# Kernel optimization log

Measured on AMD Instinct MI355X. Metric: run time of the kernel, lower is better.

## Reference

```python
import jax, jax.numpy as jnp
import numpy as np

N = 100000
E = 1600000
NFEAT, NHID, NCLASS = 128, 64, 40
EPS = 1e-5


def _sage_conv(x, src, dst, wl, wr, b):
    # mean aggregation over in-neighbors: out[dst] = mean_{src->dst} x[src]
    msg = jax.ops.segment_sum(x[src], dst, num_segments=N)          # [N, d]
    deg = jax.ops.segment_sum(jnp.ones((src.shape[0],), x.dtype), dst, num_segments=N)
    agg = msg / jnp.maximum(deg, 1.0)[:, None]
    return agg @ wl + x @ wr + b


def _bn_eval(x, g, b, m, v):
    return (x - m) * (g * jax.lax.rsqrt(v + EPS)) + b


def setup_inputs() -> dict:
    key = jax.random.key(0)
    ks = jax.random.split(key, 12)
    s = 0.05
    x = jax.random.normal(ks[0], (N, NFEAT), dtype=jnp.float32)
    edge_index = jax.random.randint(ks[1], (2, E), 0, N, dtype=jnp.int64)
    inp = {
        'x': x,
        'edge_index': edge_index,
        'w1l': jax.random.normal(ks[2], (NFEAT, NHID), jnp.float32) * s,
        'w1r': jax.random.normal(ks[3], (NFEAT, NHID), jnp.float32) * s,
        'b1': jnp.zeros((NHID,), jnp.float32),
        'wxl': jax.random.normal(ks[4], (NHID, NHID), jnp.float32) * s,
        'wxr': jax.random.normal(ks[5], (NHID, NHID), jnp.float32) * s,
        'bx': jnp.zeros((NHID,), jnp.float32),
        'w2l': jax.random.normal(ks[6], (NHID, NCLASS), jnp.float32) * s,
        'w2r': jax.random.normal(ks[7], (NHID, NCLASS), jnp.float32) * s,
        'b2': jnp.zeros((NCLASS,), jnp.float32),
        'bn3_g': jnp.ones((NHID,), jnp.float32),
        'bn3_b': jnp.zeros((NHID,), jnp.float32),
        'bn3_m': jax.random.normal(ks[8], (NHID,), jnp.float32) * 0.1,
        'bn3_v': jax.random.uniform(ks[9], (NHID,), jnp.float32, 0.5, 1.5),
        'bn2_g': jnp.ones((NCLASS,), jnp.float32),
        'bn2_b': jnp.zeros((NCLASS,), jnp.float32),
        'bn2_m': jax.random.normal(ks[10], (NCLASS,), jnp.float32) * 0.1,
        'bn2_v': jax.random.uniform(ks[11], (NCLASS,), jnp.float32, 0.5, 1.5),
    }
    return inp


def reference(x, edge_index, w1l, w1r, b1, wxl, wxr, bx, w2l, w2r, b2,
              bn3_g, bn3_b, bn3_m, bn3_v, bn2_g, bn2_b, bn2_m, bn2_v):
    src, dst = edge_index[0], edge_index[1]
    h = jax.nn.relu(_sage_conv(x, src, dst, w1l, w1r, b1))          # conv1 + relu
    # middle layer (layer=3 -> one convx iteration); dropout = identity (eval)
    h = _sage_conv(h, src, dst, wxl, wxr, bx)
    h = jax.nn.relu(_bn_eval(h, bn3_g, bn3_b, bn3_m, bn3_v))
    # final layer
    h = _sage_conv(h, src, dst, w2l, w2r, b2)
    return _bn_eval(h, bn2_g, bn2_b, bn2_m, bn2_v)                  # [N, NCLASS]
```

## Files before the change

kernel.cpp:

```cpp
#include <hip/hip_runtime.h>

#define NNODES 100000
#define NEDGES 1600000
#define NBK    196
#define BK_CAP 9000
#define BKP    17024
#define CHUNK  4096
#define ZOFF   (NNODES * 128)

typedef short bhalf8 __attribute__((ext_vector_type(8)));
typedef float f32x4 __attribute__((ext_vector_type(4)));

__device__ __forceinline__ unsigned fbits(float x){ union{float f;unsigned u;}c; c.f=x; return c.u; }
__device__ __forceinline__ float bcast(unsigned u){ union{float f;unsigned u;}c; c.u=u; return c.f; }
__device__ __forceinline__ unsigned short rtn16(float x){
    unsigned u = fbits(x);
    return (unsigned short)((u + 0x7FFFu + ((u >> 16) & 1u)) >> 16);
}

__global__ __launch_bounds__(256) void bucketize(
    const int* __restrict__ ei, unsigned* __restrict__ recs, int* __restrict__ bcur) {
    __shared__ int s_is64;
    __shared__ int cnt[256], base[256], loc[256], rnk[256];
    __shared__ unsigned stage[CHUNK];
    __shared__ unsigned char bkof[CHUNK];
    const int t = threadIdx.x;
    if (t < 64) {
        int v = ei[2 * t + 1];
        unsigned long long nz = __ballot(v != 0);
        if (t == 0) s_is64 = (nz == 0ULL) ? 1 : 0;
    }
    cnt[t] = 0; rnk[t] = 0;
    __syncthreads();
    const int is64 = s_is64;
    const long start = (long)blockIdx.x * CHUNK;
    const int2* ei2 = (const int2*)ei;
#pragma unroll
    for (int k = 0; k < CHUNK / 256; ++k) {
        long e = start + k * 256 + t;
        if (e < NEDGES) {
            int d = is64 ? ei2[NEDGES + e].x : ei[NEDGES + e];
            atomicAdd(&cnt[d >> 9], 1);
        }
    }
    __syncthreads();
    int v = cnt[t];
    int run = v;
    loc[t] = run;
    __syncthreads();
    for (int off = 1; off < 256; off <<= 1) {
        int other = (t >= off) ? loc[t - off] : 0;
        __syncthreads();
        run += other;
        loc[t] = run;
        __syncthreads();
    }
    int excl = run - v;
    if (v > 0) base[t] = atomicAdd(&bcur[t], v);
    loc[t] = excl;
    __syncthreads();
#pragma unroll
    for (int k = 0; k < CHUNK / 256; ++k) {
        long e = start + k * 256 + t;
        if (e < NEDGES) {
            int s = is64 ? ei2[e].x : ei[e];
            int d = is64 ? ei2[NEDGES + e].x : ei[NEDGES + e];
            int b = d >> 9;
            int r = atomicAdd(&rnk[b], 1);
            int pos = loc[b] + r;
            stage[pos] = ((unsigned)s << 9) | (unsigned)(d & 511);
            bkof[pos] = (unsigned char)b;
        }
    }
    __syncthreads();
    const int tot = (int)min((long)CHUNK, NEDGES - start);
    for (int i = t; i < tot; i += 256) {
        int b = bkof[i];
        int pos = base[b] + (i - loc[b]);
        if (pos < BK_CAP)
            recs[(size_t)b * BK_CAP + pos] = stage[i];
    }
}

__global__ __launch_bounds__(512) void csr_build(
    const unsigned* __restrict__ recs, const int* __restrict__ bcur,
    int2* __restrict__ offs2, int* __restrict__ degs, int* __restrict__ csr) {
    const int b = blockIdx.x;
    const int t = threadIdx.x;
    const int lo = b << 9;
    __shared__ int sc[512];
    __shared__ int hist[512];
    __shared__ int lstart[512];
    const int n = bcur[b];
    const unsigned* P = recs + (size_t)b * BK_CAP;
    hist[t] = 0;
    __syncthreads();
    for (int i = t; i < n; i += 512)
        atomicAdd(&hist[P[i] & 511], 1);
    __syncthreads();
    const int deg = hist[t];
    const int pad = (deg + 15) & ~15;
    int run = pad;
    sc[t] = run;
    __syncthreads();
    for (int off = 1; off < 512; off <<= 1) {
        int other = (t >= off) ? sc[t - off] : 0;
        __syncthreads();
        run += other;
        sc[t] = run;
        __syncthreads();
    }
    const int start = b * BKP + (run - pad);
    lstart[t] = start;
    const int node = lo + t;
    if (node < NNODES) {
        offs2[node] = make_int2(start, start + pad);
        degs[node] = deg;
    }
    hist[t] = 0;
    __syncthreads();
    for (int i = t; i < n; i += 512) {
        unsigned rec = P[i];
        int d = rec & 511;
        int r = atomicAdd(&hist[d], 1);
        csr[lstart[d] + r] = (int)(rec >> 9) * 128;
    }
    __syncthreads();
    for (int i = deg; i < pad; ++i)
        csr[start + i] = ZOFF;
}

template <int K, int NL, int NTOT>
__device__ __forceinline__ void prep_section(
    int blk, int nblk, const float* wl, const float* wr, const float* bias,
    const float* g, const float* bb, const float* m, const float* vv,
    unsigned short* Bh, unsigned short* Bl, float* bfix) {
    constexpr int NCT = NTOT / 16;
    constexpr int TOT = (K / 32) * NCT * 512;
    int tid = blk * 256 + threadIdx.x;
    if (tid < NL) {
        float sc = g ? g[tid] * rsqrtf(vv[tid] + 1e-5f) : 1.f;
        float sh = g ? (bb[tid] - m[tid] * sc) : 0.f;
        bfix[tid] = bias[tid] * sc + sh;
    }
    for (int idx = tid; idx < TOT; idx += nblk * 256) {
        int e = idx & 7, l = (idx >> 3) & 63, rest = idx >> 9;
        int ct = rest % NCT, kc = rest / NCT;
        int k = kc * 32 + (l >> 4) * 8 + e;
        int j = ct * 16 + (l & 15);
        int jj = (j < NL) ? j : j - NL;
        float sc = g ? g[jj] * rsqrtf(vv[jj] + 1e-5f) : 1.f;
        float v = ((j < NL) ? wl[k * NL + j] : wr[k * NL + (j - NL)]) * sc;
        unsigned short h = rtn16(v);
        float r1 = v - bcast((unsigned)h << 16);
        Bh[idx] = h;
        Bl[idx] = rtn16(r1);
    }
}

__global__ __launch_bounds__(256) void prep_all(
    const float* w1l, const float* w1r, const float* b1,
    const float* wxl, const float* wxr, const float* bx,
    const float* w2l, const float* w2r, const float* b2,
    const float* g3, const float* bb3, const float* m3, const float* v3,
    const float* g2, const float* bb2, const float* m2, const float* v2,
    unsigned short* B1h, unsigned short* B1l, float* bf1,
    unsigned short* B2h, unsigned short* B2l, float* bf2,
    unsigned short* B3h, unsigned short* B3l, float* bf3) {
    int blk = blockIdx.x;
    if (blk < 64)
        prep_section<128, 64, 128>(blk, 64, w1l, w1r, b1,
                                   nullptr, nullptr, nullptr, nullptr, B1h, B1l, bf1);
    else if (blk < 96)
        prep_section<64, 64, 128>(blk - 64, 32, wxl, wxr, bx,
                                  g3, bb3, m3, v3, B2h, B2l, bf2);
    else
        prep_section<64, 40, 80>(blk - 96, 20, w2l, w2r, b2,
                                 g2, bb2, m2, v2, B3h, B3l, bf3);
}

template <int K, int NL, int NTOT, bool ABF16>
__global__ __launch_bounds__(256) void gemm_mfma(
    const void* __restrict__ hvp, const unsigned short* __restrict__ Bh,
    const unsigned short* __restrict__ Bl, const float* __restrict__ bias,
    unsigned short* __restrict__ zl, unsigned short* __restrict__ zr, int nrows) {
    constexpr int NCT = NTOT / 16;
    constexpr int NKC = K / 32;
    int t = threadIdx.x;
    int l = t & 63, w = t >> 6;
    int rb = blockIdx.x * 64 + w * 16;
    int arow = rb + (l & 15);
    int kg = l >> 4;
    f32x4 acc[NCT];
#pragma unroll
    for (int ct = 0; ct < NCT; ++ct) acc[ct] = (f32x4){0.f, 0.f, 0.f, 0.f};
    const bool aok = (arow < nrows);
#pragma unroll
    for (int kc = 0; kc < NKC; ++kc) {
        bhalf8 ah = {0,0,0,0,0,0,0,0}, al = {0,0,0,0,0,0,0,0};
        if (ABF16) {
            const unsigned short* hr =
                (const unsigned short*)hvp + (long)arow * K + kg * 8;
            if (aok) ah = *(const bhalf8*)(hr + kc * 32);
        } else {
            const float* hr = (const float*)hvp + (long)arow * K + kg * 8;
            float4 a0 = make_float4(0.f, 0.f, 0.f, 0.f), a1 = a0;
            if (aok) {
                a0 = *(const float4*)(hr + kc * 32);
                a1 = *(const float4*)(hr + kc * 32 + 4);
            }
            float av[8] = {a0.x, a0.y, a0.z, a0.w, a1.x, a1.y, a1.z, a1.w};
#pragma unroll
            for (int e = 0; e < 8; ++e) {
                unsigned short hh = rtn16(av[e]);
                float r1 = av[e] - bcast((unsigned)hh << 16);
                ah[e] = (short)hh;
                al[e] = (short)rtn16(r1);
            }
        }
        const unsigned short* hp = Bh + (size_t)(kc * NCT) * 512 + l * 8;
        const unsigned short* lp = Bl + (size_t)(kc * NCT) * 512 + l * 8;
#pragma unroll
        for (int ct = 0; ct < NCT; ++ct) {
            bhalf8 bh = *(const bhalf8*)(hp + ct * 512);
            bhalf8 bl = *(const bhalf8*)(lp + ct * 512);
            acc[ct] = __builtin_amdgcn_mfma_f32_16x16x32_bf16(ah, bh, acc[ct], 0, 0, 0);
            acc[ct] = __builtin_amdgcn_mfma_f32_16x16x32_bf16(ah, bl, acc[ct], 0, 0, 0);
            if (!ABF16)
                acc[ct] = __builtin_amdgcn_mfma_f32_16x16x32_bf16(al, bh, acc[ct], 0, 0, 0);
        }
    }
    int orow0 = rb + kg * 4;
#pragma unroll
    for (int ct = 0; ct < NCT; ++ct) {
        int j = ct * 16 + (l & 15);
        bool isl = (j < NL);
        int cc = isl ? j : j - NL;
        float bj = isl ? 0.f : bias[cc];
#pragma unroll
        for (int r = 0; r < 4; ++r) {
            int orow = orow0 + r;
            if (orow < nrows) {
                if (isl) zl[(long)orow * 64 + cc] = rtn16(acc[ct][r]);
                else     zr[(long)orow * NL + cc] = rtn16(acc[ct][r] + bj);
            } else if (orow == nrows && isl) {
                zl[(long)orow * 64 + cc] = 0;
            }
        }
    }
}

template <int NOUT, bool RELU, typename OUTT>
__global__ __launch_bounds__(256) void combine_kernel(
    const unsigned short* __restrict__ zl, const unsigned short* __restrict__ zr,
    const int2* __restrict__ offs2, const int* __restrict__ degs,
    const int* __restrict__ csr, OUTT* __restrict__ out) {
    int wid  = (blockIdx.x * blockDim.x + threadIdx.x) >> 6;
    int lane = threadIdx.x & 63;
    if (wid >= NNODES) return;
    int q    = lane >> 5;
    int li2  = (lane & 31) * 2;
    unsigned lib = (unsigned)li2 * 2;
    const char* zlb = (const char*)zl;
    unsigned uzr = *(const unsigned*)&zr[(long)wid * NOUT + li2];
    float zr0 = bcast(uzr << 16), zr1 = bcast(uzr & 0xFFFF0000u);
    float invd = 1.f / fmaxf((float)degs[wid], 1.f);
    int2 se = offs2[wid];
    float ax = 0.f, ay = 0.f;
    for (int base = se.x; base < se.y; base += 64) {
        int c = min(64, se.y - base);
        int sv = csr[base + lane];
        for (int p0 = 0; p0 < c; p0 += 16) {
            unsigned hv[8];
#pragma unroll
            for (int j = 0; j < 8; ++j) {
                unsigned soff = (unsigned)__shfl(sv, p0 + 2 * j + q);
                hv[j] = *(const unsigned*)(zlb + soff + lib);
            }
#pragma unroll
            for (int j = 0; j < 8; ++j) {
                ax += bcast(hv[j] << 16);
                ay += bcast(hv[j] & 0xFFFF0000u);
            }
        }
    }
    ax += __shfl_xor(ax, 32);
    ay += __shfl_xor(ay, 32);
    if (q != 0 || li2 >= NOUT) return;
    float r0 = ax * invd + zr0;
    float r1 = ay * invd + zr1;
    if (RELU) { r0 = fmaxf(r0, 0.f); r1 = fmaxf(r1, 0.f); }
    if constexpr (sizeof(OUTT) == 4) {
        *(float2*)&out[(long)wid * NOUT + li2] = make_float2(r0, r1);
    } else {
        *(ushort2*)&out[(long)wid * NOUT + li2] = make_ushort2(rtn16(r0), rtn16(r1));
    }
}

extern "C" void kernel_launch(void* const* d_in, const int* in_sizes, int n_in,
                              void* d_out, int out_size, void* d_ws, size_t ws_size,
                              hipStream_t stream) {
    const float* x    = (const float*)d_in[0];
    const int*   ei   = (const int*)d_in[1];
    const float* w1l  = (const float*)d_in[2];
    const float* w1r  = (const float*)d_in[3];
    const float* b1   = (const float*)d_in[4];
    const float* wxl  = (const float*)d_in[5];
    const float* wxr  = (const float*)d_in[6];
    const float* bx   = (const float*)d_in[7];
    const float* w2l  = (const float*)d_in[8];
    const float* w2r  = (const float*)d_in[9];
    const float* b2   = (const float*)d_in[10];
    const float* bn3g = (const float*)d_in[11];
    const float* bn3b = (const float*)d_in[12];
    const float* bn3m = (const float*)d_in[13];
    const float* bn3v = (const float*)d_in[14];
    const float* bn2g = (const float*)d_in[15];
    const float* bn2b = (const float*)d_in[16];
    const float* bn2m = (const float*)d_in[17];
    const float* bn2v = (const float*)d_in[18];
    float* out = (float*)d_out;

    char* p = (char*)d_ws;
    auto alloc = [&](size_t bytes) -> void* {
        void* r = (void*)p;
        p += (bytes + 255) & ~(size_t)255;
        return r;
    };
    int*   bcur  = (int*)alloc(NBK * 4);
    int2*  offs2 = (int2*)alloc((size_t)NNODES * 8);
    int*   degs  = (int*)alloc((size_t)NNODES * 4);
    int*   csr   = (int*)alloc(((size_t)NBK * BKP + 64) * 4);
    unsigned short* h16  = (unsigned short*)alloc((size_t)NNODES * 64 * 2);
    unsigned short* zl16 = (unsigned short*)alloc((size_t)(NNODES + 1) * 64 * 2);
    unsigned short* zr16 = (unsigned short*)alloc((size_t)NNODES * 64 * 2);
    unsigned short* B1h = (unsigned short*)alloc(16384 * 2);
    unsigned short* B1l = (unsigned short*)alloc(16384 * 2);
    unsigned short* B2h = (unsigned short*)alloc(8192 * 2);
    unsigned short* B2l = (unsigned short*)alloc(8192 * 2);
    unsigned short* B3h = (unsigned short*)alloc(5120 * 2);
    unsigned short* B3l = (unsigned short*)alloc(5120 * 2);
    float* bfix1 = (float*)alloc(64 * 4);
    float* bfix2 = (float*)alloc(64 * 4);
    float* bfix3 = (float*)alloc(40 * 4);
    unsigned* recs = (unsigned*)h16;

    hipMemsetAsync(bcur, 0, NBK * 4, stream);
    bucketize<<<(NEDGES + CHUNK - 1) / CHUNK, 256, 0, stream>>>(ei, recs, bcur);
    prep_all<<<116, 256, 0, stream>>>(w1l, w1r, b1, wxl, wxr, bx, w2l, w2r, b2,
                                      bn3g, bn3b, bn3m, bn3v, bn2g, bn2b, bn2m, bn2v,
                                      B1h, B1l, bfix1, B2h, B2l, bfix2, B3h, B3l, bfix3);
    csr_build<<<NBK, 512, 0, stream>>>(recs, bcur, offs2, degs, csr);

    const int GB = (NNODES + 63) / 64;
    gemm_mfma<128, 64, 128, false><<<GB, 256, 0, stream>>>(x, B1h, B1l, bfix1, zl16, zr16, NNODES);
    combine_kernel<64, true, unsigned short><<<25000, 256, 0, stream>>>(
        zl16, zr16, offs2, degs, csr, h16);
    gemm_mfma<64, 64, 128, true><<<GB, 256, 0, stream>>>(h16, B2h, B2l, bfix2, zl16, zr16, NNODES);
    combine_kernel<64, true, unsigned short><<<25000, 256, 0, stream>>>(
        zl16, zr16, offs2, degs, csr, h16);
    gemm_mfma<64, 40, 80, true><<<GB, 256, 0, stream>>>(h16, B3h, B3l, bfix3, zl16, zr16, NNODES);
    combine_kernel<40, false, float><<<25000, 256, 0, stream>>>(
        zl16, zr16, offs2, degs, csr, out);
}
```

Measured before the change: 220.5 us.

## Stage GEMM weights in LDS, prefetch A rows, replace memset with kernel

The GEMM kernel now issues all A-row loads up front, then copies the whole hi/lo bf16 weight matrices into shared memory and reads B fragments from LDS instead of global memory inside the MFMA loop. The launch bounds now ask for two blocks per CU. The hipMemsetAsync that cleared the bucket counters is replaced by a tiny zeroing kernel to cut API/launch overhead. The LDS footprint (up to 64KB for the first layer) may limit occupancy, and each block repeats the full weight copy.

Measured after the change: 216.0 us (median of 2 runs). 1.02x faster.

```diff
diff --git a/kernel.cpp b/kernel.cpp
--- a/kernel.cpp
+++ b/kernel.cpp
@@ -16,6 +16,11 @@
 __device__ __forceinline__ unsigned short rtn16(float x){
     unsigned u = fbits(x);
     return (unsigned short)((u + 0x7FFFu + ((u >> 16) & 1u)) >> 16);
+}
+
+__global__ void zero_bcur(int* __restrict__ bcur) {
+    int t = threadIdx.x;
+    if (t < NBK) bcur[t] = 0;
 }
 
 __global__ __launch_bounds__(256) void bucketize(
@@ -180,54 +185,74 @@
 }
 
 template <int K, int NL, int NTOT, bool ABF16>
-__global__ __launch_bounds__(256) void gemm_mfma(
+__global__ __launch_bounds__(256, 2) void gemm_mfma(
     const void* __restrict__ hvp, const unsigned short* __restrict__ Bh,
     const unsigned short* __restrict__ Bl, const float* __restrict__ bias,
     unsigned short* __restrict__ zl, unsigned short* __restrict__ zr, int nrows) {
     constexpr int NCT = NTOT / 16;
     constexpr int NKC = K / 32;
+    constexpr int TOT = NKC * NCT * 512;
+    __shared__ unsigned short Bs[2 * TOT];
     int t = threadIdx.x;
     int l = t & 63, w = t >> 6;
     int rb = blockIdx.x * 64 + w * 16;
     int arow = rb + (l & 15);
     int kg = l >> 4;
-    f32x4 acc[NCT];
-#pragma unroll
-    for (int ct = 0; ct < NCT; ++ct) acc[ct] = (f32x4){0.f, 0.f, 0.f, 0.f};
     const bool aok = (arow < nrows);
+    bhalf8 ah_r[NKC], al_r[NKC];
+    float4 a0[NKC], a1[NKC];
 #pragma unroll
     for (int kc = 0; kc < NKC; ++kc) {
-        bhalf8 ah = {0,0,0,0,0,0,0,0}, al = {0,0,0,0,0,0,0,0};
         if (ABF16) {
             const unsigned short* hr =
                 (const unsigned short*)hvp + (long)arow * K + kg * 8;
-            if (aok) ah = *(const bhalf8*)(hr + kc * 32);
+            ah_r[kc] = (bhalf8){0,0,0,0,0,0,0,0};
+            if (aok) ah_r[kc] = *(const bhalf8*)(hr + kc * 32);
         } else {
             const float* hr = (const float*)hvp + (long)arow * K + kg * 8;
-            float4 a0 = make_float4(0.f, 0.f, 0.f, 0.f), a1 = a0;
+            a0[kc] = make_float4(0.f, 0.f, 0.f, 0.f); a1[kc] = a0[kc];
             if (aok) {
-                a0 = *(const float4*)(hr + kc * 32);
-                a1 = *(const float4*)(hr + kc * 32 + 4);
-            }
-            float av[8] = {a0.x, a0.y, a0.z, a0.w, a1.x, a1.y, a1.z, a1.w};
+                a0[kc] = *(const float4*)(hr + kc * 32);
+                a1[kc] = *(const float4*)(hr + kc * 32 + 4);
+            }
+        }
+    }
+    {
+        const uint4* gh = (const uint4*)Bh;
+        const uint4* gl = (const uint4*)Bl;
+        uint4* sh = (uint4*)Bs;
+        uint4* sl = (uint4*)(Bs + TOT);
+#pragma unroll 2
+        for (int i = t; i < TOT / 8; i += 256) { sh[i] = gh[i]; sl[i] = gl[i]; }
+    }
+    __syncthreads();
+    if (!ABF16) {
+#pragma unroll
+        for (int kc = 0; kc < NKC; ++kc) {
+            float av[8] = {a0[kc].x, a0[kc].y, a0[kc].z, a0[kc].w,
+                           a1[kc].x, a1[kc].y, a1[kc].z, a1[kc].w};
 #pragma unroll
             for (int e = 0; e < 8; ++e) {
                 unsigned short hh = rtn16(av[e]);
                 float r1 = av[e] - bcast((unsigned)hh << 16);
-                ah[e] = (short)hh;
-                al[e] = (short)rtn16(r1);
-            }
-        }
-        const unsigned short* hp = Bh + (size_t)(kc * NCT) * 512 + l * 8;
-        const unsigned short* lp = Bl + (size_t)(kc * NCT) * 512 + l * 8;
+                ah_r[kc][e] = (short)hh;
+                al_r[kc][e] = (short)rtn16(r1);
+            }
+        }
+    }
+    f32x4 acc[NCT];
+#pragma unroll
+    for (int ct = 0; ct < NCT; ++ct) acc[ct] = (f32x4){0.f, 0.f, 0.f, 0.f};
+#pragma unroll
+    for (int kc = 0; kc < NKC; ++kc) {
 #pragma unroll
         for (int ct = 0; ct < NCT; ++ct) {
-            bhalf8 bh = *(const bhalf8*)(hp + ct * 512);
-            bhalf8 bl = *(const bhalf8*)(lp + ct * 512);
-            acc[ct] = __builtin_amdgcn_mfma_f32_16x16x32_bf16(ah, bh, acc[ct], 0, 0, 0);
-            acc[ct] = __builtin_amdgcn_mfma_f32_16x16x32_bf16(ah, bl, acc[ct], 0, 0, 0);
+            bhalf8 bh = *(const bhalf8*)&Bs[(kc * NCT + ct) * 512 + l * 8];
+            bhalf8 bl2 = *(const bhalf8*)&Bs[TOT + (kc * NCT + ct) * 512 + l * 8];
+            acc[ct] = __builtin_amdgcn_mfma_f32_16x16x32_bf16(ah_r[kc], bh, acc[ct], 0, 0, 0);
+            acc[ct] = __builtin_amdgcn_mfma_f32_16x16x32_bf16(ah_r[kc], bl2, acc[ct], 0, 0, 0);
             if (!ABF16)
-                acc[ct] = __builtin_amdgcn_mfma_f32_16x16x32_bf16(al, bh, acc[ct], 0, 0, 0);
+                acc[ct] = __builtin_amdgcn_mfma_f32_16x16x32_bf16(al_r[kc], bh, acc[ct], 0, 0, 0);
         }
     }
     int orow0 = rb + kg * 4;
@@ -345,7 +370,7 @@
     float* bfix3 = (float*)alloc(40 * 4);
     unsigned* recs = (unsigned*)h16;
 
-    hipMemsetAsync(bcur, 0, NBK * 4, stream);
+    zero_bcur<<<1, 256, 0, stream>>>(bcur);
     bucketize<<<(NEDGES + CHUNK - 1) / CHUNK, 256, 0, stream>>>(ei, recs, bcur);
     prep_all<<<116, 256, 0, stream>>>(w1l, w1r, b1, wxl, wxr, bx, w2l, w2r, b2,
                                       bn3g, bn3b, bn3m, bn3v, bn2g, bn2b, bn2m, bn2v,
```
